# Kernel tuning notes

Hardware: AMD Instinct MI355X
Metric: run time of the kernel (lower is better)

The kernel has to match this reference:

```python
import jax, jax.numpy as jnp
import numpy as np

B, S, D, H = 2, 2048, 128, 8
HD = D // H  # 16


def setup_inputs() -> dict:
    key = jax.random.key(0)
    ks = jax.random.split(key, 12)
    rnd = lambda k, sh, sc=1.0: jax.random.normal(k, sh, dtype=jnp.float32) * sc
    uni = lambda k, sh: jax.random.uniform(k, sh, dtype=jnp.float32) * 0.1  # scaled to keep softmax unsaturated
    return dict(
        x_tgt=rnd(ks[0], (B, S, D)),
        enc_out=rnd(ks[1], (B, S, D)),
        self_wq=uni(ks[2], (D, D)),
        self_wk=uni(ks[3], (D, D)),
        self_wv=uni(ks[4], (D, D)),
        cross_wq=uni(ks[5], (D, D)),
        cross_wk=uni(ks[6], (D, D)),
        cross_wv=uni(ks[7], (D, D)),
        w1=rnd(ks[8], (D, D), 0.02), b1=jnp.zeros((D,), jnp.float32),
        w2=rnd(ks[9], (D, D), 0.02), b2=jnp.zeros((D,), jnp.float32),
        w3=rnd(ks[10], (D, 4 * D), 0.02), b3=jnp.zeros((4 * D,), jnp.float32),
        w4=rnd(ks[11], (4 * D, D), 0.02), b4=jnp.zeros((D,), jnp.float32),
        mask_src=jnp.ones((B, S), jnp.int32),
        mask_tgt=jnp.ones((B, S), jnp.int32),
    )


def _split(t):
    # faithful to torch: reshape (B,S,HD,H) then permute -> (B,H,S,HD)
    b, s, _ = t.shape
    return jnp.transpose(t.reshape(b, s, HD, H), (0, 3, 1, 2))


def _merge(t):
    # inverse: (B,H,S,HD) -> (B,S,HD,H) -> (B,S,D)
    b, _, s, _ = t.shape
    return jnp.transpose(t, (0, 2, 3, 1)).reshape(b, s, D)


def _attn(x_kv, x_q, wq, wk, wv):
    q = _split(x_q @ wq)   # (B,H,Sq,HD)
    k = _split(x_kv @ wk)  # (B,H,Sk,HD)
    v = _split(x_kv @ wv)
    scores = jnp.einsum('bhqd,bhkd->bhqk', q, k) / jnp.sqrt(jnp.float32(HD))
    p = jax.nn.softmax(scores, axis=-1)  # masked=True branch: no additive mask
    return _merge(jnp.einsum('bhqk,bhkd->bhqd', p, v))


def _layer_norm(x):
    # eps-less custom norm: (x - mean) / var, with unbiased variance (N-1)
    m = jnp.mean(x, axis=-1, keepdims=True)
    c = x - m
    var = jnp.sum(c * c, axis=-1, keepdims=True) / (D - 1)
    return c / var


def reference(x_tgt, enc_out, self_wq, self_wk, self_wv, cross_wq, cross_wk, cross_wv,
              w1, b1, w2, b2, w3, b3, w4, b4, mask_src, mask_tgt):
    # masked self-attention on target embeddings (no causal mask in source code)
    sa = _attn(x_tgt, x_tgt, self_wq, self_wk, self_wv)
    r1 = sa @ w1 + b1 + x_tgt
    # 'cross' attention: K/V from decoder input, Q from encoder output (faithful quirk)
    ca = _attn(x_tgt, enc_out, cross_wq, cross_wk, cross_wv)
    r2 = ca @ w2 + b2 + r1
    ln = _layer_norm(r2)
    h = jax.nn.relu(ln @ w3 + b3)
    return h @ w4 + b4 + r2
```

## Files before the change

### kernel.cpp

```cpp
#include <hip/hip_runtime.h>
#include <hip/hip_bf16.h>

#define BB 2
#define SS 2048
#define DD 128
#define HH 8
#define HDIM 16
#define DF 512
#define SPK 36
#define HS 520

typedef float floatx4 __attribute__((ext_vector_type(4)));
typedef float floatx16 __attribute__((ext_vector_type(16)));
typedef short frag8 __attribute__((ext_vector_type(8)));

__device__ __forceinline__ short f2bf(float x) {
  union { __hip_bfloat16 h; short s; } u;
  u.h = __float2bfloat16(x);
  return u.s;
}
__device__ __forceinline__ frag8 cvt8(const float4 a, const float4 b) {
  frag8 r;
  r[0] = f2bf(a.x); r[1] = f2bf(a.y); r[2] = f2bf(a.z); r[3] = f2bf(a.w);
  r[4] = f2bf(b.x); r[5] = f2bf(b.y); r[6] = f2bf(b.z); r[7] = f2bf(b.w);
  return r;
}

struct WSrc { const float* p[10]; };
__global__ __launch_bounds__(256) void wprep_kernel(WSrc w, short* __restrict__ dst) {
  const int wi = blockIdx.y;
  const int kshift = (wi == 9) ? 9 : 7;
  const int N = (wi == 8) ? 512 : 128;
  const int total = N << kshift;
  const int offs[10] = {0, 16384, 32768, 49152, 65536, 81920, 98304, 114688, 131072, 196608};
  const float sc = (wi == 0 || wi == 3) ? 0.25f : 1.0f;
  const float* src = w.p[wi];
  short* d = dst + offs[wi];
  const int K = 1 << kshift;
  for (int idx = blockIdx.x * 256 + threadIdx.x; idx < total; idx += gridDim.x * 256) {
    const int n = idx >> kshift, k = idx & (K - 1);
    d[idx] = f2bf(src[k * N + n] * sc);
  }
}

__global__ __launch_bounds__(64) void qkv_kernel(const float* __restrict__ x_tgt,
                                                 const float* __restrict__ enc_out,
                                                 const short* __restrict__ wt,
                                                 short* __restrict__ Qs, short* __restrict__ Ks,
                                                 short* __restrict__ Vts,
                                                 short* __restrict__ Qc, short* __restrict__ Kc,
                                                 short* __restrict__ Vtc) {
  const int lane = threadIdx.x, quad = lane >> 4, l16 = lane & 15;
  const int mbase = blockIdx.x * 16;
  const int which = blockIdx.y;
  const int kind = which % 3;
  const float* A = (which == 3) ? enc_out : x_tgt;
  const short* W = wt + which * 16384;
  short* Qb = (which < 3) ? Qs : Qc;
  short* Kb = (which < 3) ? Ks : Kc;
  short* Vtb = (which < 3) ? Vts : Vtc;

  __shared__ short sC[16 * 130];

  floatx4 acc[8];
#pragma unroll
  for (int ct = 0; ct < 8; ct++) acc[ct] = (floatx4){0.f, 0.f, 0.f, 0.f};

#pragma unroll
  for (int ks = 0; ks < 4; ks++) {
    const float4* ar = (const float4*)&A[(size_t)(mbase + l16) * DD + ks * 32 + quad * 8];
    const frag8 af = cvt8(ar[0], ar[1]);
#pragma unroll
    for (int ct = 0; ct < 8; ct++) {
      const frag8 bf = *(const frag8*)&W[(ct * 16 + l16) * DD + ks * 32 + quad * 8];
      acc[ct] = __builtin_amdgcn_mfma_f32_16x16x32_bf16(af, bf, acc[ct], 0, 0, 0);
    }
  }

#pragma unroll
  for (int ct = 0; ct < 8; ct++) {
#pragma unroll
    for (int r = 0; r < 4; r++) {
      sC[(quad * 4 + r) * 130 + ct * 16 + l16] = f2bf(acc[ct][r]);
    }
  }

  const int b = mbase >> 11;
  const int sbase = mbase & 2047;
  if (kind <= 1) {
    short* Dst = (kind == 0) ? Qb : Kb;
    const int s = lane >> 2, c4 = lane & 3;
#pragma unroll
    for (int h = 0; h < 8; h++) {
      short4 v;
      v.x = sC[s * 130 + (c4 * 4 + 0) * 8 + h];
      v.y = sC[s * 130 + (c4 * 4 + 1) * 8 + h];
      v.z = sC[s * 130 + (c4 * 4 + 2) * 8 + h];
      v.w = sC[s * 130 + (c4 * 4 + 3) * 8 + h];
      const int bh = b * HH + h;
      *(short4*)&Dst[((size_t)bh * SS + sbase + s) * HDIM + c4 * 4] = v;
    }
  } else {
    const int dci = lane >> 2, c4 = lane & 3;
#pragma unroll
    for (int h = 0; h < 8; h++) {
      short4 v;
      v.x = sC[(c4 * 4 + 0) * 130 + dci * 8 + h];
      v.y = sC[(c4 * 4 + 1) * 130 + dci * 8 + h];
      v.z = sC[(c4 * 4 + 2) * 130 + dci * 8 + h];
      v.w = sC[(c4 * 4 + 3) * 130 + dci * 8 + h];
      const int bh = b * HH + h;
      *(short4*)&Vtb[((size_t)bh * HDIM + dci) * SS + sbase + c4 * 4] = v;
    }
  }
}

__global__ __launch_bounds__(256) void attn_mfma_kernel(
    const short* __restrict__ Qa, const short* __restrict__ Ka,
    const short* __restrict__ Vta, short* __restrict__ AMa,
    const short* __restrict__ Qc, const short* __restrict__ Kc,
    const short* __restrict__ Vtc, short* __restrict__ AMc) {
  const int t = threadIdx.x, wid = t >> 6, lane = t & 63;
  const int l32 = lane & 31, half = lane >> 5;
  const int quad = (lane >> 4) & 3, l16 = lane & 15;
  const int bh = blockIdx.y;
  const int qbase = blockIdx.x * 32;
  const int inst = blockIdx.z;
  const short* Q = inst ? Qc : Qa;
  const short* K = inst ? Kc : Ka;
  const short* Vt = inst ? Vtc : Vta;
  short* AM = inst ? AMc : AMa;
  const size_t headoff = (size_t)bh * SS;

  __shared__ short sP[4][32 * SPK];
  __shared__ float pnum[4][16 * 33];
  __shared__ float pl[4][32];

  const frag8 qf = *(const frag8*)&Q[(headoff + qbase + l32) * HDIM + half * 8];

  frag8 onef;
#pragma unroll
  for (int i = 0; i < 8; i++) onef[i] = (short)0x3f80;

  floatx4 acc_o[2], acc_l[2];
  acc_o[0] = (floatx4){0.f, 0.f, 0.f, 0.f}; acc_o[1] = acc_o[0];
  acc_l[0] = acc_o[0]; acc_l[1] = acc_o[0];

  const int keyw = wid * 512;
#pragma unroll 1
  for (int it = 0; it < 16; it++) {
    const int kb = keyw + it * 32;
    const frag8 kf = *(const frag8*)&K[(headoff + kb + l32) * HDIM + half * 8];
    const floatx16 z16 = {0.f};
    const floatx16 sc = __builtin_amdgcn_mfma_f32_32x32x16_bf16(kf, qf, z16, 0, 0, 0);
#pragma unroll
    for (int g = 0; g < 4; g++) {
      short4 pk;
      pk.x = f2bf(__expf(sc[4 * g + 0]));
      pk.y = f2bf(__expf(sc[4 * g + 1]));
      pk.z = f2bf(__expf(sc[4 * g + 2]));
      pk.w = f2bf(__expf(sc[4 * g + 3]));
      *(short4*)&sP[wid][l32 * SPK + g * 8 + half * 4] = pk;
    }
#pragma unroll
    for (int qh = 0; qh < 2; qh++) {
      const frag8 pf = *(const frag8*)&sP[wid][(qh * 16 + l16) * SPK + quad * 8];
      const frag8 vf = *(const frag8*)&Vt[((size_t)bh * HDIM + l16) * SS + kb + quad * 8];
      acc_o[qh] = __builtin_amdgcn_mfma_f32_16x16x32_bf16(vf, pf, acc_o[qh], 0, 0, 0);
      acc_l[qh] = __builtin_amdgcn_mfma_f32_16x16x32_bf16(onef, pf, acc_l[qh], 0, 0, 0);
    }
  }

#pragma unroll
  for (int qh = 0; qh < 2; qh++) {
#pragma unroll
    for (int r = 0; r < 4; r++) {
      pnum[wid][(quad * 4 + r) * 33 + qh * 16 + l16] = acc_o[qh][r];
    }
    if (quad == 0) pl[wid][qh * 16 + l16] = acc_l[qh][0];
  }
  __syncthreads();

  {
    const int b = bh >> 3, h = bh & 7;
#pragma unroll
    for (int idx = t; idx < 512; idx += 256) {
      const int q16 = idx & 31, d = idx >> 5;
      const float num = pnum[0][d * 33 + q16] + pnum[1][d * 33 + q16] +
                        pnum[2][d * 33 + q16] + pnum[3][d * 33 + q16];
      const float l = pl[0][q16] + pl[1][q16] + pl[2][q16] + pl[3][q16];
      AM[((size_t)b * SS + qbase + q16) * DD + d * 8 + h] = f2bf(num / l);
    }
  }
}

__global__ __launch_bounds__(256) void gemm12_norm_kernel(
    const short* __restrict__ AMs, const short* __restrict__ AMc,
    const short* __restrict__ W1, const short* __restrict__ W2,
    const float* __restrict__ b1, const float* __restrict__ b2,
    const float* __restrict__ x_tgt, float* __restrict__ R2,
    short* __restrict__ LN) {
  const int t = threadIdx.x, w = t >> 6, lane = t & 63;
  const int quad = lane >> 4, l16 = lane & 15;
  const int mbase = blockIdx.x * 16;

  __shared__ float sumS[4][16];
  __shared__ float sumQ[4][16];

  floatx4 acc[2];
  acc[0] = (floatx4){0.f, 0.f, 0.f, 0.f};
  acc[1] = (floatx4){0.f, 0.f, 0.f, 0.f};

#pragma unroll
  for (int ks = 0; ks < 4; ks++) {
    const frag8 afS = *(const frag8*)&AMs[(size_t)(mbase + l16) * DD + ks * 32 + quad * 8];
    const frag8 afC = *(const frag8*)&AMc[(size_t)(mbase + l16) * DD + ks * 32 + quad * 8];
#pragma unroll
    for (int c = 0; c < 2; c++) {
      const int n0 = (w * 2 + c) * 16 + l16;
      const frag8 bf1 = *(const frag8*)&W1[n0 * DD + ks * 32 + quad * 8];
      const frag8 bf2 = *(const frag8*)&W2[n0 * DD + ks * 32 + quad * 8];
      acc[c] = __builtin_amdgcn_mfma_f32_16x16x32_bf16(afS, bf1, acc[c], 0, 0, 0);
      acc[c] = __builtin_amdgcn_mfma_f32_16x16x32_bf16(afC, bf2, acc[c], 0, 0, 0);
    }
  }

  float v[2][4];
#pragma unroll
  for (int c = 0; c < 2; c++) {
    const int n = w * 32 + c * 16 + l16;
    const float bn = b1[n] + b2[n];
#pragma unroll
    for (int r = 0; r < 4; r++) {
      const int m = mbase + quad * 4 + r;
      v[c][r] = acc[c][r] + bn + x_tgt[(size_t)m * DD + n];
      R2[(size_t)m * DD + n] = v[c][r];
    }
  }

#pragma unroll
  for (int r = 0; r < 4; r++) {
    float s = v[0][r] + v[1][r];
    float sq = v[0][r] * v[0][r] + v[1][r] * v[1][r];
#pragma unroll
    for (int mk = 1; mk < 16; mk <<= 1) {
      s += __shfl_xor(s, mk, 64);
      sq += __shfl_xor(sq, mk, 64);
    }
    if (l16 == 0) {
      sumS[w][quad * 4 + r] = s;
      sumQ[w][quad * 4 + r] = sq;
    }
  }
  __syncthreads();

#pragma unroll
  for (int r = 0; r < 4; r++) {
    const int row = quad * 4 + r;
    const float S = sumS[0][row] + sumS[1][row] + sumS[2][row] + sumS[3][row];
    const float Qs_ = sumQ[0][row] + sumQ[1][row] + sumQ[2][row] + sumQ[3][row];
    const float mean = S * (1.0f / 128.0f);
    const float cs = Qs_ - S * mean;
    const float ivar = 127.0f / cs;
    const int m = mbase + row;
#pragma unroll
    for (int c = 0; c < 2; c++) {
      const int n = w * 32 + c * 16 + l16;
      LN[(size_t)m * DD + n] = f2bf((v[c][r] - mean) * ivar);
    }
  }
}

__global__ __launch_bounds__(256) void ffn_fused_kernel(
    const short* __restrict__ LN, const short* __restrict__ W3,
    const float* __restrict__ b3, const short* __restrict__ W4,
    const float* __restrict__ b4, const float* __restrict__ R2,
    float* __restrict__ Out) {
  const int t = threadIdx.x, w = t >> 6, lane = t & 63;
  const int quad = lane >> 4, l16 = lane & 15;
  const int mbase = blockIdx.x * 16;

  __shared__ short hs[16 * HS];

  {
    floatx4 acc[8];
#pragma unroll
    for (int ct = 0; ct < 8; ct++) acc[ct] = (floatx4){0.f, 0.f, 0.f, 0.f};
    const int nblk = w * 128;
#pragma unroll
    for (int ks = 0; ks < 4; ks++) {
      const frag8 af = *(const frag8*)&LN[(size_t)(mbase + l16) * DD + ks * 32 + quad * 8];
#pragma unroll
      for (int ct = 0; ct < 8; ct++) {
        const frag8 bf = *(const frag8*)&W3[(size_t)(nblk + ct * 16 + l16) * DD + ks * 32 + quad * 8];
        acc[ct] = __builtin_amdgcn_mfma_f32_16x16x32_bf16(af, bf, acc[ct], 0, 0, 0);
      }
    }
#pragma unroll
    for (int ct = 0; ct < 8; ct++) {
      const int n = nblk + ct * 16 + l16;
      const float bn = b3[n];
#pragma unroll
      for (int r = 0; r < 4; r++) {
        hs[(quad * 4 + r) * HS + n] = f2bf(fmaxf(acc[ct][r] + bn, 0.f));
      }
    }
  }
  __syncthreads();

  {
    floatx4 acc[2];
    acc[0] = (floatx4){0.f, 0.f, 0.f, 0.f};
    acc[1] = (floatx4){0.f, 0.f, 0.f, 0.f};
#pragma unroll 4
    for (int ks = 0; ks < 16; ks++) {
      const frag8 af = *(const frag8*)&hs[l16 * HS + ks * 32 + quad * 8];
#pragma unroll
      for (int c = 0; c < 2; c++) {
        const int n0 = w * 32 + c * 16 + l16;
        const frag8 bf = *(const frag8*)&W4[(size_t)n0 * DF + ks * 32 + quad * 8];
        acc[c] = __builtin_amdgcn_mfma_f32_16x16x32_bf16(af, bf, acc[c], 0, 0, 0);
      }
    }
#pragma unroll
    for (int c = 0; c < 2; c++) {
      const int n = w * 32 + c * 16 + l16;
      const float bn = b4[n];
#pragma unroll
      for (int r = 0; r < 4; r++) {
        const int m = mbase + quad * 4 + r;
        Out[(size_t)m * DD + n] = acc[c][r] + bn + R2[(size_t)m * DD + n];
      }
    }
  }
}

extern "C" void kernel_launch(void* const* d_in, const int* in_sizes, int n_in,
                              void* d_out, int out_size, void* d_ws, size_t ws_size,
                              hipStream_t stream) {
  (void)in_sizes; (void)n_in; (void)out_size; (void)ws_size;
  const float* x_tgt   = (const float*)d_in[0];
  const float* enc_out = (const float*)d_in[1];
  const float* b1 = (const float*)d_in[9];
  const float* b2 = (const float*)d_in[11];
  const float* b3 = (const float*)d_in[13];
  const float* b4 = (const float*)d_in[15];

  WSrc wsrc;
  wsrc.p[0] = (const float*)d_in[2];
  wsrc.p[1] = (const float*)d_in[3];
  wsrc.p[2] = (const float*)d_in[4];
  wsrc.p[3] = (const float*)d_in[5];
  wsrc.p[4] = (const float*)d_in[6];
  wsrc.p[5] = (const float*)d_in[7];
  wsrc.p[6] = (const float*)d_in[8];
  wsrc.p[7] = (const float*)d_in[10];
  wsrc.p[8] = (const float*)d_in[12];
  wsrc.p[9] = (const float*)d_in[14];

  float* ws = (float*)d_ws;
  short* wt   = (short*)(ws + 0);
  short* Qs   = (short*)(ws + 131072);
  short* Ks   = (short*)(ws + 393216);
  short* Vts  = (short*)(ws + 655360);
  short* AMs  = (short*)(ws + 917504);
  short* Qc   = (short*)(ws + 1179648);
  short* Kc   = (short*)(ws + 1441792);
  short* Vtc  = (short*)(ws + 1703936);
  short* AMc  = (short*)(ws + 1966080);
  float* R2   = ws + 2228224;
  short* LN   = (short*)(ws + 2752512);

  const int M = BB * SS;
  const int MT = M / 16;

  wprep_kernel<<<dim3(64, 10), 256, 0, stream>>>(wsrc, wt);

  qkv_kernel<<<dim3(MT, 6), 64, 0, stream>>>(x_tgt, enc_out, wt, Qs, Ks, Vts, Qc, Kc, Vtc);

  attn_mfma_kernel<<<dim3(SS / 32, BB * HH, 2), 256, 0, stream>>>(
      Qs, Ks, Vts, AMs, Qc, Kc, Vtc, AMc);

  gemm12_norm_kernel<<<MT, 256, 0, stream>>>(AMs, AMc, wt + 98304, wt + 114688,
                                             b1, b2, x_tgt, R2, LN);

  ffn_fused_kernel<<<MT, 256, 0, stream>>>(LN, wt + 131072, b3, wt + 196608, b4,
                                           R2, (float*)d_out);
}
```

Baseline: 155.2 us.

## Fuse output-projection/layernorm with FFN and fold log2e into Q weights

Merges the gemm12_norm and ffn kernels into a single tail kernel. The layernorm output now stays in shared memory and the residual r2 stays in registers, so the R2 and LN global round trips and one launch go away. Separately, the Q weight scale now includes log2(e) so the attention softmax can call exp2f instead of __expf, which saves a multiply per score. The fused kernel uses more shared memory and has a longer serial chain per block, which may lower occupancy.

```diff
diff --git a/kernel.cpp b/kernel.cpp
--- a/kernel.cpp
+++ b/kernel.cpp
@@ -9,6 +9,7 @@
 #define DF 512
 #define SPK 36
 #define HS 520
+#define LNS 136
 
 typedef float floatx4 __attribute__((ext_vector_type(4)));
 typedef float floatx16 __attribute__((ext_vector_type(16)));
@@ -33,7 +34,7 @@
   const int N = (wi == 8) ? 512 : 128;
   const int total = N << kshift;
   const int offs[10] = {0, 16384, 32768, 49152, 65536, 81920, 98304, 114688, 131072, 196608};
-  const float sc = (wi == 0 || wi == 3) ? 0.25f : 1.0f;
+  const float sc = (wi == 0 || wi == 3) ? 0.25f * 1.4426950408889634f : 1.0f;
   const float* src = w.p[wi];
   short* d = dst + offs[wi];
   const int K = 1 << kshift;
@@ -156,10 +157,10 @@
 #pragma unroll
     for (int g = 0; g < 4; g++) {
       short4 pk;
-      pk.x = f2bf(__expf(sc[4 * g + 0]));
-      pk.y = f2bf(__expf(sc[4 * g + 1]));
-      pk.z = f2bf(__expf(sc[4 * g + 2]));
-      pk.w = f2bf(__expf(sc[4 * g + 3]));
+      pk.x = f2bf(exp2f(sc[4 * g + 0]));
+      pk.y = f2bf(exp2f(sc[4 * g + 1]));
+      pk.z = f2bf(exp2f(sc[4 * g + 2]));
+      pk.w = f2bf(exp2f(sc[4 * g + 3]));
       *(short4*)&sP[wid][l32 * SPK + g * 8 + half * 4] = pk;
     }
 #pragma unroll
@@ -194,23 +195,26 @@
   }
 }
 
-__global__ __launch_bounds__(256) void gemm12_norm_kernel(
+__global__ __launch_bounds__(256) void tail_kernel(
     const short* __restrict__ AMs, const short* __restrict__ AMc,
     const short* __restrict__ W1, const short* __restrict__ W2,
     const float* __restrict__ b1, const float* __restrict__ b2,
-    const float* __restrict__ x_tgt, float* __restrict__ R2,
-    short* __restrict__ LN) {
+    const float* __restrict__ x_tgt,
+    const short* __restrict__ W3, const float* __restrict__ b3,
+    const short* __restrict__ W4, const float* __restrict__ b4,
+    float* __restrict__ Out) {
   const int t = threadIdx.x, w = t >> 6, lane = t & 63;
   const int quad = lane >> 4, l16 = lane & 15;
   const int mbase = blockIdx.x * 16;
 
   __shared__ float sumS[4][16];
   __shared__ float sumQ[4][16];
-
-  floatx4 acc[2];
-  acc[0] = (floatx4){0.f, 0.f, 0.f, 0.f};
-  acc[1] = (floatx4){0.f, 0.f, 0.f, 0.f};
-
+  __shared__ short sLN[16 * LNS];
+  __shared__ short hs[16 * HS];
+
+  floatx4 acc2[2];
+  acc2[0] = (floatx4){0.f, 0.f, 0.f, 0.f};
+  acc2[1] = (floatx4){0.f, 0.f, 0.f, 0.f};
 #pragma unroll
   for (int ks = 0; ks < 4; ks++) {
     const frag8 afS = *(const frag8*)&AMs[(size_t)(mbase + l16) * DD + ks * 32 + quad * 8];
@@ -220,8 +224,8 @@
       const int n0 = (w * 2 + c) * 16 + l16;
       const frag8 bf1 = *(const frag8*)&W1[n0 * DD + ks * 32 + quad * 8];
       const frag8 bf2 = *(const frag8*)&W2[n0 * DD + ks * 32 + quad * 8];
-      acc[c] = __builtin_amdgcn_mfma_f32_16x16x32_bf16(afS, bf1, acc[c], 0, 0, 0);
-      acc[c] = __builtin_amdgcn_mfma_f32_16x16x32_bf16(afC, bf2, acc[c], 0, 0, 0);
+      acc2[c] = __builtin_amdgcn_mfma_f32_16x16x32_bf16(afS, bf1, acc2[c], 0, 0, 0);
+      acc2[c] = __builtin_amdgcn_mfma_f32_16x16x32_bf16(afC, bf2, acc2[c], 0, 0, 0);
     }
   }
 
@@ -233,8 +237,7 @@
 #pragma unroll
     for (int r = 0; r < 4; r++) {
       const int m = mbase + quad * 4 + r;
-      v[c][r] = acc[c][r] + bn + x_tgt[(size_t)m * DD + n];
-      R2[(size_t)m * DD + n] = v[c][r];
+      v[c][r] = acc2[c][r] + bn + x_tgt[(size_t)m * DD + n];
     }
   }
 
@@ -262,25 +265,13 @@
     const float mean = S * (1.0f / 128.0f);
     const float cs = Qs_ - S * mean;
     const float ivar = 127.0f / cs;
-    const int m = mbase + row;
 #pragma unroll
     for (int c = 0; c < 2; c++) {
       const int n = w * 32 + c * 16 + l16;
-      LN[(size_t)m * DD + n] = f2bf((v[c][r] - mean) * ivar);
-    }
-  }
-}
-
-__global__ __launch_bounds__(256) void ffn_fused_kernel(
-    const short* __restrict__ LN, const short* __restrict__ W3,
-    const float* __restrict__ b3, const short* __restrict__ W4,
-    const float* __restrict__ b4, const float* __restrict__ R2,
-    float* __restrict__ Out) {
-  const int t = threadIdx.x, w = t >> 6, lane = t & 63;
-  const int quad = lane >> 4, l16 = lane & 15;
-  const int mbase = blockIdx.x * 16;
-
-  __shared__ short hs[16 * HS];
+      sLN[row * LNS + n] = f2bf((v[c][r] - mean) * ivar);
+    }
+  }
+  __syncthreads();
 
   {
     floatx4 acc[8];
@@ -289,7 +280,7 @@
     const int nblk = w * 128;
 #pragma unroll
     for (int ks = 0; ks < 4; ks++) {
-      const frag8 af = *(const frag8*)&LN[(size_t)(mbase + l16) * DD + ks * 32 + quad * 8];
+      const frag8 af = *(const frag8*)&sLN[l16 * LNS + ks * 32 + quad * 8];
 #pragma unroll
       for (int ct = 0; ct < 8; ct++) {
         const frag8 bf = *(const frag8*)&W3[(size_t)(nblk + ct * 16 + l16) * DD + ks * 32 + quad * 8];
@@ -329,7 +320,7 @@
 #pragma unroll
       for (int r = 0; r < 4; r++) {
         const int m = mbase + quad * 4 + r;
-        Out[(size_t)m * DD + n] = acc[c][r] + bn + R2[(size_t)m * DD + n];
+        Out[(size_t)m * DD + n] = acc[c][r] + bn + v[c][r];
       }
     }
   }
@@ -368,8 +359,6 @@
   short* Kc   = (short*)(ws + 1441792);
   short* Vtc  = (short*)(ws + 1703936);
   short* AMc  = (short*)(ws + 1966080);
-  float* R2   = ws + 2228224;
-  short* LN   = (short*)(ws + 2752512);
 
   const int M = BB * SS;
   const int MT = M / 16;
@@ -381,9 +370,7 @@
   attn_mfma_kernel<<<dim3(SS / 32, BB * HH, 2), 256, 0, stream>>>(
       Qs, Ks, Vts, AMs, Qc, Kc, Vtc, AMc);
 
-  gemm12_norm_kernel<<<MT, 256, 0, stream>>>(AMs, AMc, wt + 98304, wt + 114688,
-                                             b1, b2, x_tgt, R2, LN);
-
-  ffn_fused_kernel<<<MT, 256, 0, stream>>>(LN, wt + 131072, b3, wt + 196608, b4,
-                                           R2, (float*)d_out);
-}
+  tail_kernel<<<MT, 256, 0, stream>>>(AMs, AMc, wt + 98304, wt + 114688,
+                                      b1, b2, x_tgt, wt + 131072, b3,
+                                      wt + 196608, b4, (float*)d_out);
+}
```

Result: slower. 161.2 us (+3.9%).
